# Kernel optimization log

Measured on AMD Instinct MI355X. Metric: run time of the kernel, lower is better.

Reference implementation:

```python
import jax, jax.numpy as jnp
import numpy as np

EPS_D = 1e-05
EPS_LOG = 1e-05
H_BAND = 0.5


def setup_inputs() -> dict:
    key = jax.random.key(0)
    k1, k2 = jax.random.split(key)
    N, C, Hh, Ww = 4, 256, 64, 64
    y = jax.random.normal(k1, (N, C, Hh, Ww), dtype=jnp.float32)
    y_hat = jax.random.normal(k2, (N, C, Hh, Ww), dtype=jnp.float32)
    return {"y": y, "y_hat": y_hat}


def contextual_loss(x, y, h=H_BAND):
    # x, y: (N, C, H, W)
    N, C, Hh, Ww = x.shape
    # mean over W, H, N of y -> per-channel mu, broadcast as (1, C, 1, 1)
    y_mu = y.mean(axis=3).mean(axis=2).mean(axis=0).reshape(1, C, 1, 1)
    x_c = x - y_mu
    y_c = y - y_mu
    x_n = x_c / jnp.linalg.norm(x_c, ord=2, axis=1, keepdims=True)
    y_n = y_c / jnp.linalg.norm(y_c, ord=2, axis=1, keepdims=True)
    x_n = x_n.reshape(N, C, Hh * Ww)  # (N, C, P)
    y_n = y_n.reshape(N, C, Hh * Ww)
    # cosine similarity: (N, P, P)
    cosine_sim = jnp.einsum('ncp,ncq->npq', x_n, y_n)
    d = 1.0 - cosine_sim
    d_min = jnp.min(d, axis=2, keepdims=True)
    d_tilde = d / (d_min + EPS_D)
    w = jnp.exp((1.0 - d_tilde) / h)
    cx_ij = w / jnp.sum(w, axis=2, keepdims=True)
    cx = jnp.mean(jnp.max(cx_ij, axis=1), axis=1)  # (N,)
    return jnp.mean(-jnp.log(cx + EPS_LOG))


def reference(y, y_hat):
    return contextual_loss(y, y_hat)
```

## Files before the change

### kernel.cpp

```cpp
#include <hip/hip_runtime.h>
#include <hip/hip_bf16.h>
#include <math.h>


namespace {
constexpr int NB = 4;
constexpr int C  = 256;
constexpr int P  = 4096;
constexpr float EPSD = 1e-5f;
constexpr float EPSL = 1e-5f;
constexpr float HB   = 0.5f;

constexpr size_t OFF_MU    = 0;
constexpr size_t OFF_XNT   = 256;
constexpr size_t OFF_YNT   = OFF_XNT + (size_t)NB * P * C / 2;
constexpr size_t OFF_XS    = OFF_YNT + (size_t)NB * P * C / 2;
constexpr size_t OFF_RMAXH = OFF_XS + (size_t)NB * P * C / 2;
constexpr size_t OFF_SUMH  = OFF_RMAXH + (size_t)NB * 4 * P;
constexpr size_t OFF_CMAXH = OFF_SUMH + (size_t)NB * 4 * P;
constexpr size_t OFF_RMAX  = OFF_CMAXH + (size_t)NB * 4 * P;
constexpr size_t OFF_ALPHA = OFF_RMAX + (size_t)NB * P;
constexpr size_t OFF_LROW  = OFF_ALPHA + (size_t)NB * P;
}

typedef __attribute__((ext_vector_type(8))) __bf16 bf16x8;
typedef __attribute__((ext_vector_type(16))) float f32x16;
typedef unsigned short u16;

__device__ __forceinline__ bf16x8 ldfrag(const u16* p) {
  return *reinterpret_cast<const bf16x8*>(p);
}
__device__ __forceinline__ void gload_lds16(const u16* g, u16* l) {
  __builtin_amdgcn_global_load_lds(
      (const __attribute__((address_space(1))) void*)g,
      (__attribute__((address_space(3))) void*)l, 16, 0, 0);
}
__device__ __forceinline__ f32x16 zero16() {
  f32x16 z;
#pragma unroll
  for (int i = 0; i < 16; ++i) z[i] = 0.f;
  return z;
}

__device__ __forceinline__ void stage_tile64(const u16* __restrict__ src, int row0,
                                             u16* lds, int t) {
#pragma unroll
  for (int i = 0; i < 4; ++i) {
    const int g  = i * 512 + t;
    const int r  = g >> 5;
    const int gs = (g & 31) ^ (r & 15);
    gload_lds16(src + (size_t)(row0 + r) * 256 + gs * 8, lds + (size_t)g * 8);
  }
}

__global__ void k_mu(const float* __restrict__ yh, float* __restrict__ ws) {
  const int c = blockIdx.x;
  const int t = threadIdx.x;
  float s = 0.f;
  for (int n = 0; n < NB; ++n) {
    const float* base = yh + ((size_t)(n * C + c)) * P;
    for (int p = t; p < P; p += 256) s += base[p];
  }
  __shared__ float red[256];
  red[t] = s;
  __syncthreads();
  for (int w = 128; w > 0; w >>= 1) {
    if (t < w) red[t] += red[t + w];
    __syncthreads();
  }
  if (t == 0) ws[OFF_MU + c] = red[0] * (1.0f / (NB * P));
}

__global__ __launch_bounds__(256) void k_norm(const float* __restrict__ x,
                                              const float* __restrict__ yh,
                                              float* __restrict__ ws) {
  const int b     = blockIdx.x;
  const int arr   = b & 1;
  const int strip = (b >> 1) & 63;
  const int n     = b >> 7;
  const int t     = threadIdx.x;
  const int w     = t >> 6;
  const int l     = t & 63;

  __shared__ float mu_s[C];
  __shared__ float tile[64][257];
  __shared__ float red[4][64];
  __shared__ float invs[64];

  mu_s[t] = ws[OFF_MU + t];
  __syncthreads();

  const float* src = arr ? yh : x;
  const size_t base = ((size_t)n * C) * P + (size_t)strip * 64 + l;
  float ssq = 0.f;
  for (int cc = 0; cc < C; cc += 4) {
    const int c = cc + w;
    const float v = src[base + (size_t)c * P] - mu_s[c];
    tile[l][c] = v;
    ssq += v * v;
  }
  red[w][l] = ssq;
  __syncthreads();
  if (t < 64) invs[t] = 1.0f / sqrtf(red[0][t] + red[1][t] + red[2][t] + red[3][t]);
  __syncthreads();

  uint* dst = reinterpret_cast<uint*>(ws + (arr ? OFF_YNT : OFF_XNT));
  const int c2 = t & 127;
  const size_t drow = ((size_t)n * P + (size_t)strip * 64) * (C / 2);
  for (int it = 0; it < 32; ++it) {
    const int pl = it * 2 + (t >> 7);
    const float s  = invs[pl];
    const float v0 = tile[pl][2 * c2] * s;
    const float v1 = tile[pl][2 * c2 + 1] * s;
    const unsigned short u0 = __builtin_bit_cast(unsigned short, __float2bfloat16(v0));
    const unsigned short u1 = __builtin_bit_cast(unsigned short, __float2bfloat16(v1));
    dst[drow + (size_t)pl * (C / 2) + c2] = ((uint)u1 << 16) | u0;
  }
}

template <int PASS>
__global__ __launch_bounds__(512, 1) void k_rows(float* __restrict__ ws) {
  const int t = threadIdx.x;
  const int wave = t >> 6, l = t & 63, l31 = l & 31, lh = l >> 5, l15 = l31 & 15;
  const int rtg = wave >> 1, ct = wave & 1;
  const int bid = blockIdx.x;
  const int qp = bid & 3, n = (bid >> 2) & 3, strip = bid >> 4;
  const int p0 = strip * 256;
  const int qbase = qp * 1024;

  const u16* A = reinterpret_cast<const u16*>(ws + (PASS == 0 ? OFF_XNT : OFF_XS)) +
                 (size_t)n * P * C;
  const u16* yn = reinterpret_cast<const u16*>(ws + OFF_YNT) + (size_t)n * P * C;

  __shared__ __align__(16) u16 Bl[3][64 * 256];
  __shared__ float red[8][64];

  const u16* Ap0 = A + (size_t)(p0 + rtg * 64 + l31) * 256;
  bf16x8 af0[16], af1[16];
#pragma unroll
  for (int ks = 0; ks < 16; ++ks) {
    af0[ks] = ldfrag(Ap0 + (ks * 2 + lh) * 8);
    af1[ks] = ldfrag(Ap0 + 32 * 256 + (ks * 2 + lh) * 8);
  }

  float arm0[16], arm1[16];
  if (PASS == 1) {
#pragma unroll
    for (int r = 0; r < 16; ++r) {
      const int row = (r & 3) + 8 * (r >> 2) + 4 * lh;
      const int pA = p0 + rtg * 64 + row;
      arm0[r] = ws[OFF_ALPHA + (size_t)n * P + pA] * ws[OFF_RMAX + (size_t)n * P + pA];
      arm1[r] = ws[OFF_ALPHA + (size_t)n * P + pA + 32] * ws[OFF_RMAX + (size_t)n * P + pA + 32];
    }
  }

  float run0[16], run1[16];
#pragma unroll
  for (int r = 0; r < 16; ++r) {
    run0[r] = (PASS == 0) ? -3.0e38f : 0.f;
    run1[r] = (PASS == 0) ? -3.0e38f : 0.f;
  }

  stage_tile64(yn, qbase, Bl[0], t);
  stage_tile64(yn, qbase + 64, Bl[1], t);

  int cur = 0;
  for (int step = 0; step < 16; ++step) {
    if (step < 15) {
      asm volatile("s_waitcnt vmcnt(4)" ::: "memory");
    } else {
      asm volatile("s_waitcnt vmcnt(0)" ::: "memory");
    }
    __builtin_amdgcn_sched_barrier(0);
    __builtin_amdgcn_s_barrier();
    __builtin_amdgcn_sched_barrier(0);
    if (step + 2 < 16) {
      const int nb = (cur == 0) ? 2 : cur - 1;
      stage_tile64(yn, qbase + (step + 2) * 64, Bl[nb], t);
    }

    const u16* Brow = &Bl[cur][(size_t)(ct * 32 + l31) * 256];
    f32x16 a0 = zero16(), a1 = zero16();
    __builtin_amdgcn_s_setprio(1);
#pragma unroll
    for (int ks = 0; ks < 16; ++ks) {
      const bf16x8 bq = ldfrag(Brow + ((ks * 2 + lh) ^ l15) * 8);
      a0 = __builtin_amdgcn_mfma_f32_32x32x16_bf16(af0[ks], bq, a0, 0, 0, 0);
      a1 = __builtin_amdgcn_mfma_f32_32x32x16_bf16(af1[ks], bq, a1, 0, 0, 0);
    }
    __builtin_amdgcn_s_setprio(0);

    if (PASS == 0) {
#pragma unroll
      for (int r = 0; r < 16; ++r) {
        run0[r] = fmaxf(run0[r], a0[r]);
        run1[r] = fmaxf(run1[r], a1[r]);
      }
    } else {
#pragma unroll
      for (int r = 0; r < 16; ++r) {
        run0[r] += __expf(a0[r] - arm0[r]);
        run1[r] += __expf(a1[r] - arm1[r]);
      }
    }
    cur = (cur == 2) ? 0 : cur + 1;
  }

#pragma unroll
  for (int m = 1; m <= 16; m <<= 1) {
#pragma unroll
    for (int r = 0; r < 16; ++r) {
      const float o0 = __shfl_xor(run0[r], m, 64);
      const float o1 = __shfl_xor(run1[r], m, 64);
      run0[r] = (PASS == 0) ? fmaxf(run0[r], o0) : (run0[r] + o0);
      run1[r] = (PASS == 0) ? fmaxf(run1[r], o1) : (run1[r] + o1);
    }
  }
  if (l31 == 0) {
#pragma unroll
    for (int r = 0; r < 16; ++r) {
      const int row = (r & 3) + 8 * (r >> 2) + 4 * lh;
      red[wave][row]      = run0[r];
      red[wave][row + 32] = run1[r];
    }
  }
  __syncthreads();
  if (t < 256) {
    const int rtg2 = t >> 6, row = t & 63;
    const float v0 = red[rtg2 * 2][row], v1 = red[rtg2 * 2 + 1][row];
    const size_t o = (size_t)(n * 4 + qp) * P + p0 + rtg2 * 64 + row;
    if (PASS == 0)
      ws[OFF_RMAXH + o] = fmaxf(v0, v1);
    else
      ws[OFF_SUMH + o] = v0 + v1;
  }
}

__global__ void k_alpha(float* __restrict__ ws) {
  const int i = blockIdx.x * 256 + threadIdx.x;
  const int n = i >> 12, p = i & (P - 1);
  float rm = ws[OFF_RMAXH + (size_t)(n * 4) * P + p];
#pragma unroll
  for (int j = 1; j < 4; ++j)
    rm = fmaxf(rm, ws[OFF_RMAXH + (size_t)(n * 4 + j) * P + p]);
  ws[OFF_RMAX + (size_t)n * P + p]  = rm;
  ws[OFF_ALPHA + (size_t)n * P + p] = 1.0f / (HB * (1.0f - rm + EPSD));
}

__global__ __launch_bounds__(256) void k_scale(float* __restrict__ ws) {
  const int g = blockIdx.x * 256 + threadIdx.x;
  const int rowg = g >> 5;
  const int n = rowg >> 12, p = rowg & (P - 1);
  const float a = ws[OFF_ALPHA + (size_t)n * P + p];
  const uint4 v = reinterpret_cast<const uint4*>(ws + OFF_XNT)[g];
  uint4 o;
  uint* vi = (uint*)&v;
  uint* oi = (uint*)&o;
#pragma unroll
  for (int j = 0; j < 4; ++j) {
    const uint u = vi[j];
    const float f0 = __builtin_bit_cast(float, (u & 0xffffu) << 16) * a;
    const float f1 = __builtin_bit_cast(float, (u & 0xffff0000u)) * a;
    const unsigned short b0 = __builtin_bit_cast(unsigned short, __float2bfloat16(f0));
    const unsigned short b1 = __builtin_bit_cast(unsigned short, __float2bfloat16(f1));
    oi[j] = ((uint)b1 << 16) | b0;
  }
  reinterpret_cast<uint4*>(ws + OFF_XS)[g] = o;
}

__global__ void k_L(float* __restrict__ ws) {
  const int i = blockIdx.x * 256 + threadIdx.x;
  const int n = i >> 12, p = i & (P - 1);
  float s = 0.f;
#pragma unroll
  for (int j = 0; j < 4; ++j)
    s += ws[OFF_SUMH + (size_t)(n * 4 + j) * P + p];
  const float a_ = ws[OFF_ALPHA + (size_t)n * P + p];
  const float rm = ws[OFF_RMAX + (size_t)n * P + p];
  ws[OFF_LROW + (size_t)n * P + p] = fmaf(a_, rm, logf(s));
}

__global__ __launch_bounds__(512, 1) void k_colp(float* __restrict__ ws) {
  const int t = threadIdx.x;
  const int wave = t >> 6, l = t & 63, l31 = l & 31, lh = l >> 5, l15 = l31 & 15;
  const int rtg = wave >> 1, ct = wave & 1;
  const int bid = blockIdx.x;
  const int pp = bid & 3, n = (bid >> 2) & 3, qstrip = bid >> 4;
  const int q0 = qstrip * 256;
  const int pbase = pp * 1024;

  const u16* yn = reinterpret_cast<const u16*>(ws + OFF_YNT) + (size_t)n * P * C;
  const u16* xs = reinterpret_cast<const u16*>(ws + OFF_XS) + (size_t)n * P * C;
  const float* lrw = ws + OFF_LROW + (size_t)n * P;

  __shared__ __align__(16) u16 Bl[3][64 * 256];
  __shared__ float red[8][64];

  const u16* Ap0 = yn + (size_t)(q0 + rtg * 64 + l31) * 256;
  bf16x8 af0[16], af1[16];
#pragma unroll
  for (int ks = 0; ks < 16; ++ks) {
    af0[ks] = ldfrag(Ap0 + (ks * 2 + lh) * 8);
    af1[ks] = ldfrag(Ap0 + 32 * 256 + (ks * 2 + lh) * 8);
  }

  float run0[16], run1[16];
#pragma unroll
  for (int r = 0; r < 16; ++r) { run0[r] = -3.0e38f; run1[r] = -3.0e38f; }

  stage_tile64(xs, pbase, Bl[0], t);
  stage_tile64(xs, pbase + 64, Bl[1], t);

  int cur = 0;
  for (int step = 0; step < 16; ++step) {
    if (step < 15) {
      asm volatile("s_waitcnt vmcnt(4)" ::: "memory");
    } else {
      asm volatile("s_waitcnt vmcnt(0)" ::: "memory");
    }
    __builtin_amdgcn_sched_barrier(0);
    __builtin_amdgcn_s_barrier();
    __builtin_amdgcn_sched_barrier(0);
    if (step + 2 < 16) {
      const int nb = (cur == 0) ? 2 : cur - 1;
      stage_tile64(xs, pbase + (step + 2) * 64, Bl[nb], t);
    }

    const float L_ = lrw[pbase + step * 64 + ct * 32 + l31];

    const u16* Brow = &Bl[cur][(size_t)(ct * 32 + l31) * 256];
    f32x16 a0 = zero16(), a1 = zero16();
    __builtin_amdgcn_s_setprio(1);
#pragma unroll
    for (int ks = 0; ks < 16; ++ks) {
      const bf16x8 bq = ldfrag(Brow + ((ks * 2 + lh) ^ l15) * 8);
      a0 = __builtin_amdgcn_mfma_f32_32x32x16_bf16(af0[ks], bq, a0, 0, 0, 0);
      a1 = __builtin_amdgcn_mfma_f32_32x32x16_bf16(af1[ks], bq, a1, 0, 0, 0);
    }
    __builtin_amdgcn_s_setprio(0);
#pragma unroll
    for (int r = 0; r < 16; ++r) {
      run0[r] = fmaxf(run0[r], a0[r] - L_);
      run1[r] = fmaxf(run1[r], a1[r] - L_);
    }
    cur = (cur == 2) ? 0 : cur + 1;
  }

#pragma unroll
  for (int m = 1; m <= 16; m <<= 1) {
#pragma unroll
    for (int r = 0; r < 16; ++r) {
      run0[r] = fmaxf(run0[r], __shfl_xor(run0[r], m, 64));
      run1[r] = fmaxf(run1[r], __shfl_xor(run1[r], m, 64));
    }
  }
  if (l31 == 0) {
#pragma unroll
    for (int r = 0; r < 16; ++r) {
      const int row = (r & 3) + 8 * (r >> 2) + 4 * lh;
      red[wave][row]      = run0[r];
      red[wave][row + 32] = run1[r];
    }
  }
  __syncthreads();
  if (t < 256) {
    const int rtg2 = t >> 6, row = t & 63;
    const float v = fmaxf(red[rtg2 * 2][row], red[rtg2 * 2 + 1][row]);
    ws[OFF_CMAXH + (size_t)(n * 4 + pp) * P + q0 + rtg2 * 64 + row] = v;
  }
}

__global__ void k_final(const float* __restrict__ ws, float* __restrict__ out) {
  const int t = threadIdx.x;
  __shared__ float red[256];
  __shared__ float lsum_s;
  if (t == 0) lsum_s = 0.f;
  for (int n = 0; n < NB; ++n) {
    float e = 0.f;
    for (int q = t; q < P; q += 256) {
      float m = ws[OFF_CMAXH + (size_t)(n * 4) * P + q];
#pragma unroll
      for (int j = 1; j < 4; ++j)
        m = fmaxf(m, ws[OFF_CMAXH + (size_t)(n * 4 + j) * P + q]);
      e += __expf(m);
    }
    __syncthreads();
    red[t] = e;
    __syncthreads();
    for (int w = 128; w > 0; w >>= 1) {
      if (t < w) red[t] += red[t + w];
      __syncthreads();
    }
    if (t == 0) lsum_s += -logf(red[0] * (1.0f / P) + EPSL);
  }
  __syncthreads();
  if (t == 0) out[0] = lsum_s * 0.25f;
}

extern "C" void kernel_launch(void* const* d_in, const int* in_sizes, int n_in,
                              void* d_out, int out_size, void* d_ws, size_t ws_size,
                              hipStream_t stream) {
  const float* x  = (const float*)d_in[0];
  const float* yh = (const float*)d_in[1];
  float* ws  = (float*)d_ws;
  float* out = (float*)d_out;

  k_mu<<<dim3(C), dim3(256), 0, stream>>>(yh, ws);
  k_norm<<<dim3(NB * 64 * 2), dim3(256), 0, stream>>>(x, yh, ws);
  k_rows<0><<<dim3(256), dim3(512), 0, stream>>>(ws);
  k_alpha<<<dim3(NB * P / 256), dim3(256), 0, stream>>>(ws);
  k_scale<<<dim3(NB * P * C / 8 / 256), dim3(256), 0, stream>>>(ws);
  k_rows<1><<<dim3(256), dim3(512), 0, stream>>>(ws);
  k_L<<<dim3(NB * P / 256), dim3(256), 0, stream>>>(ws);
  k_colp<<<dim3(256), dim3(512), 0, stream>>>(ws);
  k_final<<<dim3(1), dim3(256), 0, stream>>>(ws, out);
}
```

Before: 206.3 us.

## Retile similarity GEMM kernels to 128-row blocks and drop the row-max shift

Restructures k_rows and k_colp to use 256-thread blocks that each own 128 rows and sweep half of the opposite dimension, instead of 512-thread blocks owning 256 rows over a quarter. All partial-result buffers and the reduce kernels shrink from 4 to 2 splits. The second pass now sums exp of the raw scaled similarity and k_L keeps only log(sum), which removes the per-row alpha*rmax shift. k_colp also stages its log-row values in LDS, and the setprio hints are removed. The price is fewer waves per CU, twice as much streaming of B tiles per output row, and possible exp overflow when alpha*rmax is large.

Measured after the change: 216.3 us. 1.05x slower.

```diff
diff --git a/kernel.cpp b/kernel.cpp
--- a/kernel.cpp
+++ b/kernel.cpp
@@ -16,9 +16,9 @@
 constexpr size_t OFF_YNT   = OFF_XNT + (size_t)NB * P * C / 2;
 constexpr size_t OFF_XS    = OFF_YNT + (size_t)NB * P * C / 2;
 constexpr size_t OFF_RMAXH = OFF_XS + (size_t)NB * P * C / 2;
-constexpr size_t OFF_SUMH  = OFF_RMAXH + (size_t)NB * 4 * P;
-constexpr size_t OFF_CMAXH = OFF_SUMH + (size_t)NB * 4 * P;
-constexpr size_t OFF_RMAX  = OFF_CMAXH + (size_t)NB * 4 * P;
+constexpr size_t OFF_SUMH  = OFF_RMAXH + (size_t)NB * 2 * P;
+constexpr size_t OFF_CMAXH = OFF_SUMH + (size_t)NB * 2 * P;
+constexpr size_t OFF_RMAX  = OFF_CMAXH + (size_t)NB * 2 * P;
 constexpr size_t OFF_ALPHA = OFF_RMAX + (size_t)NB * P;
 constexpr size_t OFF_LROW  = OFF_ALPHA + (size_t)NB * P;
 }
@@ -45,8 +45,8 @@
 __device__ __forceinline__ void stage_tile64(const u16* __restrict__ src, int row0,
                                              u16* lds, int t) {
 #pragma unroll
-  for (int i = 0; i < 4; ++i) {
-    const int g  = i * 512 + t;
+  for (int i = 0; i < 8; ++i) {
+    const int g  = i * 256 + t;
     const int r  = g >> 5;
     const int gs = (g & 31) ^ (r & 15);
     gload_lds16(src + (size_t)(row0 + r) * 256 + gs * 8, lds + (size_t)g * 8);
@@ -119,23 +119,23 @@
 }
 
 template <int PASS>
-__global__ __launch_bounds__(512, 1) void k_rows(float* __restrict__ ws) {
+__global__ __launch_bounds__(256, 1) void k_rows(float* __restrict__ ws) {
   const int t = threadIdx.x;
   const int wave = t >> 6, l = t & 63, l31 = l & 31, lh = l >> 5, l15 = l31 & 15;
-  const int rtg = wave >> 1, ct = wave & 1;
+  const int rt = wave >> 1, ct = wave & 1;
   const int bid = blockIdx.x;
-  const int qp = bid & 3, n = (bid >> 2) & 3, strip = bid >> 4;
-  const int p0 = strip * 256;
-  const int qbase = qp * 1024;
+  const int qh = bid & 1, n = (bid >> 1) & 3, strip = bid >> 3;
+  const int p0 = strip * 128;
+  const int qbase = qh * 2048;
 
   const u16* A = reinterpret_cast<const u16*>(ws + (PASS == 0 ? OFF_XNT : OFF_XS)) +
                  (size_t)n * P * C;
   const u16* yn = reinterpret_cast<const u16*>(ws + OFF_YNT) + (size_t)n * P * C;
 
   __shared__ __align__(16) u16 Bl[3][64 * 256];
-  __shared__ float red[8][64];
-
-  const u16* Ap0 = A + (size_t)(p0 + rtg * 64 + l31) * 256;
+  __shared__ float red[4][64];
+
+  const u16* Ap0 = A + (size_t)(p0 + rt * 64 + l31) * 256;
   bf16x8 af0[16], af1[16];
 #pragma unroll
   for (int ks = 0; ks < 16; ++ks) {
@@ -143,17 +143,6 @@
     af1[ks] = ldfrag(Ap0 + 32 * 256 + (ks * 2 + lh) * 8);
   }
 
-  float arm0[16], arm1[16];
-  if (PASS == 1) {
-#pragma unroll
-    for (int r = 0; r < 16; ++r) {
-      const int row = (r & 3) + 8 * (r >> 2) + 4 * lh;
-      const int pA = p0 + rtg * 64 + row;
-      arm0[r] = ws[OFF_ALPHA + (size_t)n * P + pA] * ws[OFF_RMAX + (size_t)n * P + pA];
-      arm1[r] = ws[OFF_ALPHA + (size_t)n * P + pA + 32] * ws[OFF_RMAX + (size_t)n * P + pA + 32];
-    }
-  }
-
   float run0[16], run1[16];
 #pragma unroll
   for (int r = 0; r < 16; ++r) {
@@ -165,30 +154,28 @@
   stage_tile64(yn, qbase + 64, Bl[1], t);
 
   int cur = 0;
-  for (int step = 0; step < 16; ++step) {
-    if (step < 15) {
-      asm volatile("s_waitcnt vmcnt(4)" ::: "memory");
+  for (int step = 0; step < 32; ++step) {
+    if (step < 31) {
+      asm volatile("s_waitcnt vmcnt(8)" ::: "memory");
     } else {
       asm volatile("s_waitcnt vmcnt(0)" ::: "memory");
     }
     __builtin_amdgcn_sched_barrier(0);
     __builtin_amdgcn_s_barrier();
     __builtin_amdgcn_sched_barrier(0);
-    if (step + 2 < 16) {
+    if (step + 2 < 32) {
       const int nb = (cur == 0) ? 2 : cur - 1;
       stage_tile64(yn, qbase + (step + 2) * 64, Bl[nb], t);
     }
 
     const u16* Brow = &Bl[cur][(size_t)(ct * 32 + l31) * 256];
     f32x16 a0 = zero16(), a1 = zero16();
-    __builtin_amdgcn_s_setprio(1);
 #pragma unroll
     for (int ks = 0; ks < 16; ++ks) {
       const bf16x8 bq = ldfrag(Brow + ((ks * 2 + lh) ^ l15) * 8);
       a0 = __builtin_amdgcn_mfma_f32_32x32x16_bf16(af0[ks], bq, a0, 0, 0, 0);
       a1 = __builtin_amdgcn_mfma_f32_32x32x16_bf16(af1[ks], bq, a1, 0, 0, 0);
     }
-    __builtin_amdgcn_s_setprio(0);
 
     if (PASS == 0) {
 #pragma unroll
@@ -199,8 +186,8 @@
     } else {
 #pragma unroll
       for (int r = 0; r < 16; ++r) {
-        run0[r] += __expf(a0[r] - arm0[r]);
-        run1[r] += __expf(a1[r] - arm1[r]);
+        run0[r] += __expf(a0[r]);
+        run1[r] += __expf(a1[r]);
       }
     }
     cur = (cur == 2) ? 0 : cur + 1;
@@ -225,10 +212,10 @@
     }
   }
   __syncthreads();
-  if (t < 256) {
-    const int rtg2 = t >> 6, row = t & 63;
-    const float v0 = red[rtg2 * 2][row], v1 = red[rtg2 * 2 + 1][row];
-    const size_t o = (size_t)(n * 4 + qp) * P + p0 + rtg2 * 64 + row;
+  if (t < 128) {
+    const int rt2 = t >> 6, row = t & 63;
+    const float v0 = red[rt2 * 2][row], v1 = red[rt2 * 2 + 1][row];
+    const size_t o = (size_t)(n * 2 + qh) * P + p0 + rt2 * 64 + row;
     if (PASS == 0)
       ws[OFF_RMAXH + o] = fmaxf(v0, v1);
     else
@@ -239,10 +226,8 @@
 __global__ void k_alpha(float* __restrict__ ws) {
   const int i = blockIdx.x * 256 + threadIdx.x;
   const int n = i >> 12, p = i & (P - 1);
-  float rm = ws[OFF_RMAXH + (size_t)(n * 4) * P + p];
-#pragma unroll
-  for (int j = 1; j < 4; ++j)
-    rm = fmaxf(rm, ws[OFF_RMAXH + (size_t)(n * 4 + j) * P + p]);
+  const float rm = fmaxf(ws[OFF_RMAXH + (size_t)(n * 2) * P + p],
+                         ws[OFF_RMAXH + (size_t)(n * 2 + 1) * P + p]);
   ws[OFF_RMAX + (size_t)n * P + p]  = rm;
   ws[OFF_ALPHA + (size_t)n * P + p] = 1.0f / (HB * (1.0f - rm + EPSD));
 }
@@ -271,32 +256,29 @@
 __global__ void k_L(float* __restrict__ ws) {
   const int i = blockIdx.x * 256 + threadIdx.x;
   const int n = i >> 12, p = i & (P - 1);
-  float s = 0.f;
-#pragma unroll
-  for (int j = 0; j < 4; ++j)
-    s += ws[OFF_SUMH + (size_t)(n * 4 + j) * P + p];
-  const float a_ = ws[OFF_ALPHA + (size_t)n * P + p];
-  const float rm = ws[OFF_RMAX + (size_t)n * P + p];
-  ws[OFF_LROW + (size_t)n * P + p] = fmaf(a_, rm, logf(s));
-}
-
-__global__ __launch_bounds__(512, 1) void k_colp(float* __restrict__ ws) {
+  const float s = ws[OFF_SUMH + (size_t)(n * 2) * P + p] +
+                  ws[OFF_SUMH + (size_t)(n * 2 + 1) * P + p];
+  ws[OFF_LROW + (size_t)n * P + p] = logf(s);
+}
+
+__global__ __launch_bounds__(256, 1) void k_colp(float* __restrict__ ws) {
   const int t = threadIdx.x;
   const int wave = t >> 6, l = t & 63, l31 = l & 31, lh = l >> 5, l15 = l31 & 15;
-  const int rtg = wave >> 1, ct = wave & 1;
+  const int rt = wave >> 1, ct = wave & 1;
   const int bid = blockIdx.x;
-  const int pp = bid & 3, n = (bid >> 2) & 3, qstrip = bid >> 4;
-  const int q0 = qstrip * 256;
-  const int pbase = pp * 1024;
+  const int ph = bid & 1, n = (bid >> 1) & 3, qstrip = bid >> 3;
+  const int q0 = qstrip * 128;
+  const int pbase = ph * 2048;
 
   const u16* yn = reinterpret_cast<const u16*>(ws + OFF_YNT) + (size_t)n * P * C;
   const u16* xs = reinterpret_cast<const u16*>(ws + OFF_XS) + (size_t)n * P * C;
   const float* lrw = ws + OFF_LROW + (size_t)n * P;
 
   __shared__ __align__(16) u16 Bl[3][64 * 256];
-  __shared__ float red[8][64];
-
-  const u16* Ap0 = yn + (size_t)(q0 + rtg * 64 + l31) * 256;
+  __shared__ float red[4][64];
+  __shared__ float Lsh[2048];
+
+  const u16* Ap0 = yn + (size_t)(q0 + rt * 64 + l31) * 256;
   bf16x8 af0[16], af1[16];
 #pragma unroll
   for (int ks = 0; ks < 16; ++ks) {
@@ -304,6 +286,9 @@
     af1[ks] = ldfrag(Ap0 + 32 * 256 + (ks * 2 + lh) * 8);
   }
 
+  for (int i = t; i < 2048; i += 256) Lsh[i] = lrw[pbase + i];
+  __syncthreads();
+
   float run0[16], run1[16];
 #pragma unroll
   for (int r = 0; r < 16; ++r) { run0[r] = -3.0e38f; run1[r] = -3.0e38f; }
@@ -312,32 +297,30 @@
   stage_tile64(xs, pbase + 64, Bl[1], t);
 
   int cur = 0;
-  for (int step = 0; step < 16; ++step) {
-    if (step < 15) {
-      asm volatile("s_waitcnt vmcnt(4)" ::: "memory");
+  for (int step = 0; step < 32; ++step) {
+    if (step < 31) {
+      asm volatile("s_waitcnt vmcnt(8)" ::: "memory");
     } else {
       asm volatile("s_waitcnt vmcnt(0)" ::: "memory");
     }
     __builtin_amdgcn_sched_barrier(0);
     __builtin_amdgcn_s_barrier();
     __builtin_amdgcn_sched_barrier(0);
-    if (step + 2 < 16) {
+    if (step + 2 < 32) {
       const int nb = (cur == 0) ? 2 : cur - 1;
       stage_tile64(xs, pbase + (step + 2) * 64, Bl[nb], t);
     }
 
-    const float L_ = lrw[pbase + step * 64 + ct * 32 + l31];
+    const float L_ = Lsh[step * 64 + ct * 32 + l31];
 
     const u16* Brow = &Bl[cur][(size_t)(ct * 32 + l31) * 256];
     f32x16 a0 = zero16(), a1 = zero16();
-    __builtin_amdgcn_s_setprio(1);
 #pragma unroll
     for (int ks = 0; ks < 16; ++ks) {
       const bf16x8 bq = ldfrag(Brow + ((ks * 2 + lh) ^ l15) * 8);
       a0 = __builtin_amdgcn_mfma_f32_32x32x16_bf16(af0[ks], bq, a0, 0, 0, 0);
       a1 = __builtin_amdgcn_mfma_f32_32x32x16_bf16(af1[ks], bq, a1, 0, 0, 0);
     }
-    __builtin_amdgcn_s_setprio(0);
 #pragma unroll
     for (int r = 0; r < 16; ++r) {
       run0[r] = fmaxf(run0[r], a0[r] - L_);
@@ -363,10 +346,10 @@
     }
   }
   __syncthreads();
-  if (t < 256) {
-    const int rtg2 = t >> 6, row = t & 63;
-    const float v = fmaxf(red[rtg2 * 2][row], red[rtg2 * 2 + 1][row]);
-    ws[OFF_CMAXH + (size_t)(n * 4 + pp) * P + q0 + rtg2 * 64 + row] = v;
+  if (t < 128) {
+    const int rt2 = t >> 6, row = t & 63;
+    const float v = fmaxf(red[rt2 * 2][row], red[rt2 * 2 + 1][row]);
+    ws[OFF_CMAXH + (size_t)(n * 2 + ph) * P + q0 + rt2 * 64 + row] = v;
   }
 }
 
@@ -378,10 +361,8 @@
   for (int n = 0; n < NB; ++n) {
     float e = 0.f;
     for (int q = t; q < P; q += 256) {
-      float m = ws[OFF_CMAXH + (size_t)(n * 4) * P + q];
-#pragma unroll
-      for (int j = 1; j < 4; ++j)
-        m = fmaxf(m, ws[OFF_CMAXH + (size_t)(n * 4 + j) * P + q]);
+      const float m = fmaxf(ws[OFF_CMAXH + (size_t)(n * 2) * P + q],
+                            ws[OFF_CMAXH + (size_t)(n * 2 + 1) * P + q]);
       e += __expf(m);
     }
     __syncthreads();
@@ -407,11 +388,11 @@
 
   k_mu<<<dim3(C), dim3(256), 0, stream>>>(yh, ws);
   k_norm<<<dim3(NB * 64 * 2), dim3(256), 0, stream>>>(x, yh, ws);
-  k_rows<0><<<dim3(256), dim3(512), 0, stream>>>(ws);
+  k_rows<0><<<dim3(256), dim3(256), 0, stream>>>(ws);
   k_alpha<<<dim3(NB * P / 256), dim3(256), 0, stream>>>(ws);
   k_scale<<<dim3(NB * P * C / 8 / 256), dim3(256), 0, stream>>>(ws);
-  k_rows<1><<<dim3(256), dim3(512), 0, stream>>>(ws);
+  k_rows<1><<<dim3(256), dim3(256), 0, stream>>>(ws);
   k_L<<<dim3(NB * P / 256), dim3(256), 0, stream>>>(ws);
-  k_colp<<<dim3(256), dim3(512), 0, stream>>>(ws);
+  k_colp<<<dim3(256), dim3(256), 0, stream>>>(ws);
   k_final<<<dim3(1), dim3(256), 0, stream>>>(ws, out);
 }
```
